# Optimization experiments

Measured on AMD Instinct MI355X. Metric: run time of the kernel, lower is better.

Reference implementation:

```python
import jax, jax.numpy as jnp
import numpy as np

B, T, C, H = 2, 2048, 1024, 16
D = C // H  # head dim = 64

def setup_inputs() -> dict:
    key = jax.random.key(0)
    k1, k2, k3 = jax.random.split(key, 3)
    x = jax.random.normal(k1, (B, T, C), dtype=jnp.float32)
    w_attn = jax.random.normal(k2, (C, 3 * C), dtype=jnp.float32) * (1.0 / np.sqrt(C))
    w_proj = jax.random.normal(k3, (C, C), dtype=jnp.float32) * (1.0 / np.sqrt(C))
    return {"x": x, "w_attn": w_attn, "w_proj": w_proj}

def reference(x, w_attn, w_proj):
    # qkv projection: [B,T,3C]
    qkv = jnp.einsum('btc,cd->btd', x, w_attn)
    q, k, v = jnp.split(qkv, 3, axis=-1)
    # reshape to [B,H,T,D]
    q = q.reshape(B, T, H, D).transpose(0, 2, 1, 3)
    k = k.reshape(B, T, H, D).transpose(0, 2, 1, 3)
    v = v.reshape(B, T, H, D).transpose(0, 2, 1, 3)
    scale = 1.0 / jnp.sqrt(jnp.asarray(D, dtype=q.dtype))
    att = jnp.einsum('bhqd,bhkd->bhqk', q, k) * scale  # [B,H,T,T]
    att = jax.nn.softmax(att, axis=-1)
    y = jnp.einsum('bhqk,bhkd->bhqd', att, v)  # [B,H,T,D]
    y = y.transpose(0, 2, 1, 3).reshape(B, T, C)
    return jnp.einsum('btc,cd->btd', y, w_proj)
```

## Files before the change

### kernel.cpp

```cpp
#include <hip/hip_runtime.h>
#include <hip/hip_bf16.h>


typedef unsigned short u16;
using bf16x8 = __attribute__((ext_vector_type(8))) short;
using f32x4  = __attribute__((ext_vector_type(4))) float;

#define T_SEQ 2048
#define CDIM  1024

#define QSCALE 0.18033688011112042f

#if __has_builtin(__builtin_amdgcn_exp2f)
#define EXP2(x) __builtin_amdgcn_exp2f(x)
#else
#define EXP2(x) __expf((x) * 0.6931471805599453f)
#endif

__device__ inline u16 f2bf(float f) {
  __hip_bfloat16 h = __float2bfloat16(f);
  return *reinterpret_cast<u16*>(&h);
}
__device__ inline unsigned pk2bf(float a, float b) {
  return (unsigned)f2bf(a) | ((unsigned)f2bf(b) << 16);
}

__device__ inline void gload_lds16(const u16* g, u16* l) {
  __builtin_amdgcn_global_load_lds((const __attribute__((address_space(1))) void*)g,
                                   (__attribute__((address_space(3))) void*)l, 16, 0, 0);
}

__device__ inline int swz128(int r, int c) {
  return (((r << 7) + (c << 1)) ^ ((r & 7) << 4)) >> 1;
}

__global__ __launch_bounds__(256) void conv_bf16_kernel(const float* __restrict__ in,
                                                        u16* __restrict__ out, int n4) {
  int idx = blockIdx.x * 256 + threadIdx.x;
  if (idx >= n4) return;
  float4 v = reinterpret_cast<const float4*>(in)[idx];
  ushort4 o;
  o.x = f2bf(v.x); o.y = f2bf(v.y); o.z = f2bf(v.z); o.w = f2bf(v.w);
  reinterpret_cast<ushort4*>(out)[idx] = o;
}

__global__ __launch_bounds__(256) void transp_conv_kernel(const float* __restrict__ in,
                                                          u16* __restrict__ out, int R, int N,
                                                          int scale_rows, float scale) {
  __shared__ float tile[32][33];
  int nbx = N >> 5;
  int bx = blockIdx.x % nbx, by = blockIdx.x / nbx;
  int tx = threadIdx.x & 31, ty = threadIdx.x >> 5;
#pragma unroll
  for (int rr = ty; rr < 32; rr += 8)
    tile[rr][tx] = in[(long)(by * 32 + rr) * N + bx * 32 + tx];
  __syncthreads();
#pragma unroll
  for (int rr = ty; rr < 32; rr += 8) {
    float s = (bx * 32 + rr) < scale_rows ? scale : 1.0f;
    out[(long)(bx * 32 + rr) * R + by * 32 + tx] = f2bf(tile[tx][rr] * s);
  }
}

template <bool OUT_F32>
__global__ __launch_bounds__(256) void gemm_bt_kernel(const u16* __restrict__ A,
                                                      const u16* __restrict__ Bt,
                                                      void* __restrict__ C,
                                                      int N, int K) {
  __shared__ u16 As[2][128 * 32];
  __shared__ u16 Bs[2][128 * 32];
  const int tid = threadIdx.x;
  const int lane = tid & 63, wid = tid >> 6;
  const int l16 = lane & 15, lh = lane >> 4;
  const int wm = wid >> 1, wn = wid & 1;
  const int q8 = gridDim.x >> 3;
  const int wg = (blockIdx.x & 7) * q8 + (blockIdx.x >> 3);
  const int nTn = N >> 7;
  const int tn = wg % nTn;
  const int tm = wg / nTn;

  f32x4 acc[4][4];
#pragma unroll
  for (int i = 0; i < 4; ++i)
#pragma unroll
    for (int j = 0; j < 4; ++j)
      acc[i][j] = f32x4{0.f, 0.f, 0.f, 0.f};

  const long aRow = (long)(tm * 128 + wid * 16 + (lane >> 2)) * K + (lane & 3) * 8;
  const long bRow = (long)(tn * 128 + wid * 16 + (lane >> 2)) * K + (lane & 3) * 8;
  const long rstep = (long)64 * K;
  const int ldsOff = wid * 512;

  gload_lds16(A + aRow, As[0] + ldsOff);
  gload_lds16(A + aRow + rstep, As[0] + ldsOff + 2048);
  gload_lds16(Bt + bRow, Bs[0] + ldsOff);
  gload_lds16(Bt + bRow + rstep, Bs[0] + ldsOff + 2048);
  __syncthreads();

  int cur = 0;
  for (int k0 = 0; k0 < K; k0 += 32) {
    if (k0 + 32 < K) {
      gload_lds16(A + aRow + k0 + 32, As[cur ^ 1] + ldsOff);
      gload_lds16(A + aRow + rstep + k0 + 32, As[cur ^ 1] + ldsOff + 2048);
      gload_lds16(Bt + bRow + k0 + 32, Bs[cur ^ 1] + ldsOff);
      gload_lds16(Bt + bRow + rstep + k0 + 32, Bs[cur ^ 1] + ldsOff + 2048);
    }
    bf16x8 af[4], bfr[4];
#pragma unroll
    for (int i = 0; i < 4; ++i)
      af[i] = *reinterpret_cast<const bf16x8*>(&As[cur][(wm * 64 + i * 16 + l16) * 32 + lh * 8]);
#pragma unroll
    for (int j = 0; j < 4; ++j)
      bfr[j] = *reinterpret_cast<const bf16x8*>(&Bs[cur][(wn * 64 + j * 16 + l16) * 32 + lh * 8]);
#pragma unroll
    for (int i = 0; i < 4; ++i)
#pragma unroll
      for (int j = 0; j < 4; ++j)
        acc[i][j] = __builtin_amdgcn_mfma_f32_16x16x32_bf16(af[i], bfr[j], acc[i][j], 0, 0, 0);
    __syncthreads();
    cur ^= 1;
  }

#pragma unroll
  for (int i = 0; i < 4; ++i) {
#pragma unroll
    for (int j = 0; j < 4; ++j) {
#pragma unroll
      for (int r = 0; r < 4; ++r) {
        long row = tm * 128 + wm * 64 + i * 16 + lh * 4 + r;
        long col = tn * 128 + wn * 64 + j * 16 + l16;
        if (OUT_F32)
          reinterpret_cast<float*>(C)[row * N + col] = acc[i][j][r];
        else
          reinterpret_cast<u16*>(C)[row * N + col] = f2bf(acc[i][j][r]);
      }
    }
  }
}

__global__ __launch_bounds__(256) void vtrans_kernel(const u16* __restrict__ qkv,
                                                     u16* __restrict__ vT) {
  __shared__ u16 Ts[64 * 64];
  const int tid = threadIdx.x;
  const int bid = blockIdx.x;
  const int tt = bid & 31, bh = bid >> 5;
  const int b = bh >> 4, h = bh & 15;
  const int sr = tid >> 2, sc = (tid & 3) * 16;
  const u16* src = qkv + (long)(b * T_SEQ + tt * 64 + sr) * 3072 + 2 * CDIM + h * 64 + sc;
  uint4 v0 = *reinterpret_cast<const uint4*>(src);
  uint4 v1 = *reinterpret_cast<const uint4*>(src + 8);
  *reinterpret_cast<uint4*>(&Ts[swz128(sr, sc)]) = v0;
  *reinterpret_cast<uint4*>(&Ts[swz128(sr, sc + 8)]) = v1;
  __syncthreads();
  union { uint4 u[2]; u16 s[16]; } o;
#pragma unroll
  for (int i = 0; i < 16; ++i) o.s[i] = Ts[swz128(sc + i, sr)];
  u16* dst = vT + (long)(bh * 64 + sr) * T_SEQ + tt * 64 + sc;
  reinterpret_cast<uint4*>(dst)[0] = o.u[0];
  reinterpret_cast<uint4*>(dst)[1] = o.u[1];
}

__global__ __launch_bounds__(256) void attn_kernel(const u16* __restrict__ qkv,
                                                   const u16* __restrict__ vT,
                                                   u16* __restrict__ y) {
  __shared__ u16 Qs[64 * 64];
  __shared__ u16 Ks[64 * 64];
  __shared__ u16 Vt[64 * 64];
  __shared__ u16 Ps[4][16 * 64];
  const int tid = threadIdx.x;
  const int lane = tid & 63, wid = tid >> 6;
  const int l16 = lane & 15, lh = lane >> 4;
  const int bid = blockIdx.x;
  const int qt = bid & 31, h = (bid >> 5) & 15, b = bid >> 9;

  const u16* qbase = qkv + (long)(b * T_SEQ + qt * 64) * 3072 + h * 64;
  const u16* kbase = qkv + (long)(b * T_SEQ) * 3072 + CDIM + h * 64;
  const u16* vtbase = vT + (long)((b * 16 + h) * 64) * T_SEQ;

  const int sr = tid >> 2, sc = (tid & 3) * 16;
  const int ss0 = swz128(sr, sc), ss1 = swz128(sr, sc + 8);

  int kvo[2][4];
#pragma unroll
  for (int cb = 0; cb < 4; ++cb) {
    kvo[0][cb] = swz128(cb * 16 + l16, lh * 8);
    kvo[1][cb] = swz128(cb * 16 + l16, 32 + lh * 8);
  }
  const int pxor = (l16 & 7) << 3;
  int pwi[4];
#pragma unroll
  for (int cb = 0; cb < 4; ++cb) pwi[cb] = (l16 * 64 + cb * 16 + lh * 4) ^ pxor;
  const int pri0 = (l16 * 64 + lh * 8) ^ pxor;
  const int pri1 = (l16 * 64 + 32 + lh * 8) ^ pxor;

  {
    uint4 v0 = *reinterpret_cast<const uint4*>(qbase + (long)sr * 3072 + sc);
    uint4 v1 = *reinterpret_cast<const uint4*>(qbase + (long)sr * 3072 + sc + 8);
    *reinterpret_cast<uint4*>(&Qs[ss0]) = v0;
    *reinterpret_cast<uint4*>(&Qs[ss1]) = v1;
  }
  uint4 kr0 = *reinterpret_cast<const uint4*>(kbase + (long)sr * 3072 + sc);
  uint4 kr1 = *reinterpret_cast<const uint4*>(kbase + (long)sr * 3072 + sc + 8);
  uint4 vr0 = *reinterpret_cast<const uint4*>(vtbase + (long)sr * T_SEQ + sc);
  uint4 vr1 = *reinterpret_cast<const uint4*>(vtbase + (long)sr * T_SEQ + sc + 8);

  __syncthreads();
  bf16x8 qf0 = *reinterpret_cast<const bf16x8*>(&Qs[swz128(wid * 16 + l16, lh * 8)]);
  bf16x8 qf1 = *reinterpret_cast<const bf16x8*>(&Qs[swz128(wid * 16 + l16, 32 + lh * 8)]);

  f32x4 oacc[4];
  float lp = 0.f;
#pragma unroll
  for (int cb = 0; cb < 4; ++cb) oacc[cb] = f32x4{0.f, 0.f, 0.f, 0.f};

  for (int kt = 0; kt < 32; ++kt) {
    *reinterpret_cast<uint4*>(&Ks[ss0]) = kr0;
    *reinterpret_cast<uint4*>(&Ks[ss1]) = kr1;
    *reinterpret_cast<uint4*>(&Vt[ss0]) = vr0;
    *reinterpret_cast<uint4*>(&Vt[ss1]) = vr1;
    __syncthreads();
    if (kt < 31) {
      const u16* ks = kbase + (long)((kt + 1) * 64 + sr) * 3072 + sc;
      const u16* vs = vtbase + (long)sr * T_SEQ + (kt + 1) * 64 + sc;
      kr0 = *reinterpret_cast<const uint4*>(ks);
      kr1 = *reinterpret_cast<const uint4*>(ks + 8);
      vr0 = *reinterpret_cast<const uint4*>(vs);
      vr1 = *reinterpret_cast<const uint4*>(vs + 8);
    }

    f32x4 sacc[4];
#pragma unroll
    for (int cb = 0; cb < 4; ++cb) {
      sacc[cb] = f32x4{0.f, 0.f, 0.f, 0.f};
      bf16x8 kf0 = *reinterpret_cast<const bf16x8*>(&Ks[kvo[0][cb]]);
      bf16x8 kf1 = *reinterpret_cast<const bf16x8*>(&Ks[kvo[1][cb]]);
      sacc[cb] = __builtin_amdgcn_mfma_f32_16x16x32_bf16(kf0, qf0, sacc[cb], 0, 0, 0);
      sacc[cb] = __builtin_amdgcn_mfma_f32_16x16x32_bf16(kf1, qf1, sacc[cb], 0, 0, 0);
    }

    float p[4][4];
#pragma unroll
    for (int cb = 0; cb < 4; ++cb)
#pragma unroll
      for (int r = 0; r < 4; ++r) p[cb][r] = EXP2(sacc[cb][r]);
#pragma unroll
    for (int cb = 0; cb < 4; ++cb)
      lp += (p[cb][0] + p[cb][1]) + (p[cb][2] + p[cb][3]);
#pragma unroll
    for (int cb = 0; cb < 4; ++cb) {
      uint2 w2;
      w2.x = pk2bf(p[cb][0], p[cb][1]);
      w2.y = pk2bf(p[cb][2], p[cb][3]);
      *reinterpret_cast<uint2*>(&Ps[wid][pwi[cb]]) = w2;
    }

    bf16x8 pf0 = *reinterpret_cast<const bf16x8*>(&Ps[wid][pri0]);
    bf16x8 pf1 = *reinterpret_cast<const bf16x8*>(&Ps[wid][pri1]);

#pragma unroll
    for (int cb = 0; cb < 4; ++cb) {
      bf16x8 vf0 = *reinterpret_cast<const bf16x8*>(&Vt[kvo[0][cb]]);
      bf16x8 vf1 = *reinterpret_cast<const bf16x8*>(&Vt[kvo[1][cb]]);
      oacc[cb] = __builtin_amdgcn_mfma_f32_16x16x32_bf16(vf0, pf0, oacc[cb], 0, 0, 0);
      oacc[cb] = __builtin_amdgcn_mfma_f32_16x16x32_bf16(vf1, pf1, oacc[cb], 0, 0, 0);
    }
    __syncthreads();
  }

  float s = lp;
  s += __shfl_xor(s, 16);
  s += __shfl_xor(s, 32);
  const float inv = __builtin_amdgcn_rcpf(s);

#pragma unroll
  for (int cb = 0; cb < 4; ++cb) {
    uint2 w2;
    w2.x = pk2bf(oacc[cb][0] * inv, oacc[cb][1] * inv);
    w2.y = pk2bf(oacc[cb][2] * inv, oacc[cb][3] * inv);
    *reinterpret_cast<uint2*>(&Ps[wid][pwi[cb]]) = w2;
  }
  const int er = lane >> 2, ec = lane & 3;
  const int exr = (er & 7) << 3;
  const int eri0 = (er * 64 + ec * 16) ^ exr;
  const int eri1 = (er * 64 + ec * 16 + 8) ^ exr;
  uint4 o0 = *reinterpret_cast<const uint4*>(&Ps[wid][eri0]);
  uint4 o1 = *reinterpret_cast<const uint4*>(&Ps[wid][eri1]);
  u16* yrow = y + (long)(b * T_SEQ + qt * 64 + wid * 16 + er) * CDIM + h * 64 + ec * 16;
  reinterpret_cast<uint4*>(yrow)[0] = o0;
  *reinterpret_cast<uint4*>(yrow + 8) = o1;
}

extern "C" void kernel_launch(void* const* d_in, const int* in_sizes, int n_in,
                              void* d_out, int out_size, void* d_ws, size_t ws_size,
                              hipStream_t stream) {
  const float* x      = (const float*)d_in[0];
  const float* w_attn = (const float*)d_in[1];
  const float* w_proj = (const float*)d_in[2];

  char* ws = (char*)d_ws;
  u16* xb   = (u16*)(ws + 0);
  u16* wat  = (u16*)(ws + 8388608);
  u16* wpt  = (u16*)(ws + 14680064);
  u16* qkvb = (u16*)(ws + 16777216);
  u16* yb   = (u16*)(ws + 41943040);
  u16* vT   = xb;

  conv_bf16_kernel<<<4096, 256, 0, stream>>>(x, xb, 1048576);
  transp_conv_kernel<<<96 * 32, 256, 0, stream>>>(w_attn, wat, 1024, 3072, 1024, QSCALE);
  transp_conv_kernel<<<32 * 32, 256, 0, stream>>>(w_proj, wpt, 1024, 1024, 0, 1.0f);
  gemm_bt_kernel<false><<<32 * 24, 256, 0, stream>>>(xb, wat, qkvb, 3072, 1024);
  vtrans_kernel<<<32 * 32, 256, 0, stream>>>(qkvb, vT);
  attn_kernel<<<2 * 16 * 32, 256, 0, stream>>>(qkvb, vT, yb);
  gemm_bt_kernel<true><<<32 * 8, 256, 0, stream>>>(yb, wpt, d_out, 1024, 1024);
}
```

Before: 207.0 us.

## Fuse V transpose into QKV GEMM epilogue and shrink output-projection tile width

The QKV GEMM gains a mode where blocks covering the V columns write their results directly in transposed layout into a separate vT buffer, so the standalone vtrans kernel and its global round trip are skipped whenever the workspace is large enough. The output projection GEMM now uses a 128x64 tile, doubling its block count to 512 for better CU occupancy. The XCD-aware block swizzle is replaced with a simple tm/tn mapping, which may change L2 locality. The V epilogue writes 8-byte strided stores, which may coalesce worse than the original transpose kernel.

```diff
diff --git a/kernel.cpp b/kernel.cpp
--- a/kernel.cpp
+++ b/kernel.cpp
@@ -62,39 +62,39 @@
   }
 }
 
-template <bool OUT_F32>
+template <int MODE, int BN>
 __global__ __launch_bounds__(256) void gemm_bt_kernel(const u16* __restrict__ A,
                                                       const u16* __restrict__ Bt,
                                                       void* __restrict__ C,
+                                                      u16* __restrict__ vT,
                                                       int N, int K) {
+  constexpr int NJ = BN / 32;
+  constexpr int WN = BN / 2;
   __shared__ u16 As[2][128 * 32];
-  __shared__ u16 Bs[2][128 * 32];
+  __shared__ u16 Bs[2][BN * 32];
   const int tid = threadIdx.x;
   const int lane = tid & 63, wid = tid >> 6;
   const int l16 = lane & 15, lh = lane >> 4;
   const int wm = wid >> 1, wn = wid & 1;
-  const int q8 = gridDim.x >> 3;
-  const int wg = (blockIdx.x & 7) * q8 + (blockIdx.x >> 3);
-  const int nTn = N >> 7;
-  const int tn = wg % nTn;
-  const int tm = wg / nTn;
-
-  f32x4 acc[4][4];
+  const int tm = blockIdx.x & 31;
+  const int tn = blockIdx.x >> 5;
+
+  f32x4 acc[4][NJ];
 #pragma unroll
   for (int i = 0; i < 4; ++i)
 #pragma unroll
-    for (int j = 0; j < 4; ++j)
+    for (int j = 0; j < NJ; ++j)
       acc[i][j] = f32x4{0.f, 0.f, 0.f, 0.f};
 
   const long aRow = (long)(tm * 128 + wid * 16 + (lane >> 2)) * K + (lane & 3) * 8;
-  const long bRow = (long)(tn * 128 + wid * 16 + (lane >> 2)) * K + (lane & 3) * 8;
+  const long bRow = (long)(tn * BN + wid * 16 + (lane >> 2)) * K + (lane & 3) * 8;
   const long rstep = (long)64 * K;
   const int ldsOff = wid * 512;
 
   gload_lds16(A + aRow, As[0] + ldsOff);
   gload_lds16(A + aRow + rstep, As[0] + ldsOff + 2048);
   gload_lds16(Bt + bRow, Bs[0] + ldsOff);
-  gload_lds16(Bt + bRow + rstep, Bs[0] + ldsOff + 2048);
+  if (BN == 128) gload_lds16(Bt + bRow + rstep, Bs[0] + ldsOff + 2048);
   __syncthreads();
 
   int cur = 0;
@@ -103,33 +103,52 @@
       gload_lds16(A + aRow + k0 + 32, As[cur ^ 1] + ldsOff);
       gload_lds16(A + aRow + rstep + k0 + 32, As[cur ^ 1] + ldsOff + 2048);
       gload_lds16(Bt + bRow + k0 + 32, Bs[cur ^ 1] + ldsOff);
-      gload_lds16(Bt + bRow + rstep + k0 + 32, Bs[cur ^ 1] + ldsOff + 2048);
-    }
-    bf16x8 af[4], bfr[4];
+      if (BN == 128) gload_lds16(Bt + bRow + rstep + k0 + 32, Bs[cur ^ 1] + ldsOff + 2048);
+    }
+    bf16x8 af[4], bfr[NJ];
 #pragma unroll
     for (int i = 0; i < 4; ++i)
       af[i] = *reinterpret_cast<const bf16x8*>(&As[cur][(wm * 64 + i * 16 + l16) * 32 + lh * 8]);
 #pragma unroll
-    for (int j = 0; j < 4; ++j)
-      bfr[j] = *reinterpret_cast<const bf16x8*>(&Bs[cur][(wn * 64 + j * 16 + l16) * 32 + lh * 8]);
+    for (int j = 0; j < NJ; ++j)
+      bfr[j] = *reinterpret_cast<const bf16x8*>(&Bs[cur][(wn * WN + j * 16 + l16) * 32 + lh * 8]);
 #pragma unroll
     for (int i = 0; i < 4; ++i)
 #pragma unroll
-      for (int j = 0; j < 4; ++j)
+      for (int j = 0; j < NJ; ++j)
         acc[i][j] = __builtin_amdgcn_mfma_f32_16x16x32_bf16(af[i], bfr[j], acc[i][j], 0, 0, 0);
     __syncthreads();
     cur ^= 1;
   }
 
+  if (MODE == 2 && tn >= 16) {
+    const int bsel = tm >> 4;
+    const int t0 = (tm & 15) * 128 + wm * 64 + lh * 4;
+#pragma unroll
+    for (int i = 0; i < 4; ++i) {
+#pragma unroll
+      for (int j = 0; j < NJ; ++j) {
+        const int h = 2 * (tn - 16) + wn;
+        const int d = j * 16 + l16;
+        u16* dst = vT + (long)((bsel * 16 + h) * 64 + d) * T_SEQ + t0 + i * 16;
+        uint2 w2;
+        w2.x = pk2bf(acc[i][j][0], acc[i][j][1]);
+        w2.y = pk2bf(acc[i][j][2], acc[i][j][3]);
+        *reinterpret_cast<uint2*>(dst) = w2;
+      }
+    }
+    return;
+  }
+
 #pragma unroll
   for (int i = 0; i < 4; ++i) {
 #pragma unroll
-    for (int j = 0; j < 4; ++j) {
+    for (int j = 0; j < NJ; ++j) {
 #pragma unroll
       for (int r = 0; r < 4; ++r) {
         long row = tm * 128 + wm * 64 + i * 16 + lh * 4 + r;
-        long col = tn * 128 + wn * 64 + j * 16 + l16;
-        if (OUT_F32)
+        long col = tn * BN + wn * WN + j * 16 + l16;
+        if (MODE == 1)
           reinterpret_cast<float*>(C)[row * N + col] = acc[i][j][r];
         else
           reinterpret_cast<u16*>(C)[row * N + col] = f2bf(acc[i][j][r]);
@@ -303,13 +322,19 @@
   u16* wpt  = (u16*)(ws + 14680064);
   u16* qkvb = (u16*)(ws + 16777216);
   u16* yb   = (u16*)(ws + 41943040);
-  u16* vT   = xb;
+
+  const bool fused = ws_size >= 58720256;
+  u16* vT = fused ? (u16*)(ws + 50331648) : xb;
 
   conv_bf16_kernel<<<4096, 256, 0, stream>>>(x, xb, 1048576);
   transp_conv_kernel<<<96 * 32, 256, 0, stream>>>(w_attn, wat, 1024, 3072, 1024, QSCALE);
   transp_conv_kernel<<<32 * 32, 256, 0, stream>>>(w_proj, wpt, 1024, 1024, 0, 1.0f);
-  gemm_bt_kernel<false><<<32 * 24, 256, 0, stream>>>(xb, wat, qkvb, 3072, 1024);
-  vtrans_kernel<<<32 * 32, 256, 0, stream>>>(qkvb, vT);
+  if (fused) {
+    gemm_bt_kernel<2, 128><<<32 * 24, 256, 0, stream>>>(xb, wat, qkvb, vT, 3072, 1024);
+  } else {
+    gemm_bt_kernel<0, 128><<<32 * 24, 256, 0, stream>>>(xb, wat, qkvb, nullptr, 3072, 1024);
+    vtrans_kernel<<<32 * 32, 256, 0, stream>>>(qkvb, vT);
+  }
   attn_kernel<<<2 * 16 * 32, 256, 0, stream>>>(qkvb, vT, yb);
-  gemm_bt_kernel<true><<<32 * 8, 256, 0, stream>>>(yb, wpt, d_out, 1024, 1024);
-}
+  gemm_bt_kernel<1, 64><<<32 * 16, 256, 0, stream>>>(yb, wpt, d_out, nullptr, 1024, 1024);
+}
```

New measurement: 196.6 us. -5.0%, faster.
